# Performance work log

Hardware: AMD Instinct MI355X
Metric: run time of the kernel (lower is better)

The kernel has to match this reference:

```python
import jax, jax.numpy as jnp
import numpy as np

N_NODES = 100000
N_EDGES = 1600000
N_GRAPHS = 256
HIDDEN = 128
IN_FEAT = 5


def setup_inputs() -> dict:
    key = jax.random.key(0)
    ks = jax.random.split(key, 12)
    x = jax.random.normal(ks[0], (N_NODES, IN_FEAT), dtype=jnp.float32)
    edge_index = jax.random.randint(ks[1], (2, N_EDGES), 0, N_NODES, dtype=jnp.int64)
    batch = jnp.sort(jax.random.randint(ks[2], (N_NODES,), 0, N_GRAPHS, dtype=jnp.int64))
    s = 0.05
    W0 = jax.random.normal(ks[3], (IN_FEAT, HIDDEN), dtype=jnp.float32) * s
    b0 = jnp.zeros((HIDDEN,), dtype=jnp.float32)
    W1 = jax.random.normal(ks[4], (HIDDEN, HIDDEN), dtype=jnp.float32) * s
    b1 = jnp.zeros((HIDDEN,), dtype=jnp.float32)
    W2 = jax.random.normal(ks[5], (HIDDEN, HIDDEN), dtype=jnp.float32) * s
    b2 = jnp.zeros((HIDDEN,), dtype=jnp.float32)
    lin_w = jax.random.normal(ks[6], (HIDDEN, 1), dtype=jnp.float32) * s
    lin_b = jnp.zeros((1,), dtype=jnp.float32)
    return {"x": x, "edge_index": edge_index, "batch": batch,
            "W0": W0, "b0": b0, "W1": W1, "b1": b1, "W2": W2, "b2": b2,
            "lin_w": lin_w, "lin_b": lin_b}


def reference(x, edge_index, batch, W0, b0, W1, b1, W2, b2, lin_w, lin_b):
    n = x.shape[0]
    # PyG GCNConv: add self-loops, symmetric normalization D^-1/2 (A+I) D^-1/2
    loop = jnp.arange(n, dtype=edge_index.dtype)
    src = jnp.concatenate([edge_index[0], loop])  # [E+N]
    dst = jnp.concatenate([edge_index[1], loop])
    deg = jax.ops.segment_sum(jnp.ones_like(dst, dtype=x.dtype), dst, num_segments=n)
    dis = jnp.where(deg > 0, jax.lax.rsqrt(jnp.maximum(deg, 1.0)), 0.0)
    norm = (dis[src] * dis[dst])[:, None]  # [E+N, 1]

    def gcn_conv(h, W, b):
        h = h @ W                      # [N, H]
        msg = h[src] * norm            # gather + scale, [E+N, H]
        return jax.ops.segment_sum(msg, dst, num_segments=n) + b

    h = jax.nn.relu(gcn_conv(x, W0, b0))
    h = jax.nn.relu(gcn_conv(h, W1, b1))
    h = gcn_conv(h, W2, b2)

    # global_mean_pool over batch ids
    sums = jax.ops.segment_sum(h, batch, num_segments=N_GRAPHS)
    cnt = jax.ops.segment_sum(jnp.ones((n,), x.dtype), batch, num_segments=N_GRAPHS)
    g = sums / jnp.maximum(cnt, 1.0)[:, None]
    # dropout p=0.01 is identity in eval mode
    return jax.nn.sigmoid(g @ lin_w + lin_b)  # [N_GRAPHS, 1]
```

## Files before the change

### kernel.cpp

```cpp
#include <hip/hip_runtime.h>
#include <hip/hip_fp8.h>

#define GCN_N 100000
#define GCN_H 128
#define GCN_G 256
#define NPB_SHIFT 9
#define NPB 512
#define NBKT 196
#define CHUNK 2048
#define SRC_BITS 17
#define SRC_MASK ((1 << SRC_BITS) - 1)
#define T1_SCALE 256.0f
#define T1_INV_SCALE (1.0f / 256.0f)
#define EBUF_CAP 10240

static_assert(GCN_N < (1 << SRC_BITS), "src id must fit 17 bits");

using short8 = __attribute__((ext_vector_type(8))) short;
using f32x4  = __attribute__((ext_vector_type(4))) float;
using f32x2  = __attribute__((ext_vector_type(2))) float;

#if defined(__has_builtin)
#if __has_builtin(__builtin_amdgcn_cvt_pk_f32_fp8) && __has_builtin(__builtin_amdgcn_cvt_pk_fp8_f32)
#define HW_FP8 1
#endif
#endif


__device__ __forceinline__ unsigned short f2bf(float f) {
    unsigned u = __float_as_uint(f);
    unsigned r = u + 0x7FFFu + ((u >> 16) & 1u);
    return (unsigned short)(r >> 16);
}
__device__ __forceinline__ float bf2f(unsigned short h) {
    return __uint_as_float(((unsigned)h) << 16);
}

__device__ __forceinline__ void fp8x4_to_f32(unsigned v, float* f) {
#ifdef HW_FP8
    f32x2 lo = __builtin_amdgcn_cvt_pk_f32_fp8((int)v, false);
    f32x2 hi = __builtin_amdgcn_cvt_pk_f32_fp8((int)v, true);
    f[0] = lo[0]; f[1] = lo[1]; f[2] = hi[0]; f[3] = hi[1];
#else
    #pragma unroll
    for (int j = 0; j < 4; j++) {
        __hip_fp8_e4m3 h;
        h.__x = (unsigned char)((v >> (8 * j)) & 0xFF);
        f[j] = (float)h;
    }
#endif
}

__device__ __forceinline__ unsigned f32x4_to_fp8(float f0, float f1, float f2, float f3) {
#ifdef HW_FP8
    int r = __builtin_amdgcn_cvt_pk_fp8_f32(f0, f1, 0, false);
    r = __builtin_amdgcn_cvt_pk_fp8_f32(f2, f3, r, true);
    return (unsigned)r;
#else
    unsigned r = 0;
    float ff[4] = {f0, f1, f2, f3};
    #pragma unroll
    for (int j = 0; j < 4; j++) {
        __hip_fp8_e4m3 h(ff[j]);
        r |= ((unsigned)h.__x) << (8 * j);
    }
    return r;
#endif
}


__global__ __launch_bounds__(256) void hist_kernel(const int* __restrict__ dst,
                                                   int* __restrict__ hist, int E) {
    __shared__ int lh[NBKT];
    int tid = threadIdx.x;
    if (tid < NBKT) lh[tid] = 0;
    __syncthreads();
    int e0 = blockIdx.x * CHUNK;
    #pragma unroll
    for (int i = 0; i < CHUNK / 256; i++) {
        int e = e0 + tid + i * 256;
        if (e < E) atomicAdd(&lh[dst[e] >> NPB_SHIFT], 1);
    }
    __syncthreads();
    if (tid < NBKT) hist[(size_t)blockIdx.x * NBKT + tid] = lh[tid];
}

__global__ __launch_bounds__(64) void scan_cols_kernel(const int* __restrict__ hist,
                                                       int* __restrict__ offsT,
                                                       int* __restrict__ btot, int B) {
    int k = blockIdx.x;
    int lane = threadIdx.x;
    int running = 0;
    for (int b0 = 0; b0 < B; b0 += 64) {
        int b = b0 + lane;
        int v = (b < B) ? hist[(size_t)b * NBKT + k] : 0;
        int iv = v;
        #pragma unroll
        for (int d = 1; d < 64; d <<= 1) {
            int x = __shfl_up(iv, d, 64);
            if (lane >= d) iv += x;
        }
        if (b < B) offsT[(size_t)k * B + b] = running + iv - v;
        running += __shfl(iv, 63, 64);
    }
    if (lane == 0) btot[k] = running;
}

__global__ __launch_bounds__(256) void prep_kernel(const float* __restrict__ W1,
                                                   const float* __restrict__ W2,
                                                   const float* __restrict__ b2,
                                                   const float* __restrict__ lw,
                                                   const int* __restrict__ btot,
                                                   unsigned short* __restrict__ w1t,
                                                   float* __restrict__ w2l,
                                                   float* __restrict__ c2,
                                                   int* __restrict__ bbase,
                                                   int* __restrict__ rowptr, int n) {
    __shared__ float slw[128];
    int blk = blockIdx.x, tid = threadIdx.x;
    if (blk < 64) {
        int idx = blk * 256 + tid;
        int col = idx >> 7, k = idx & 127;
        w1t[idx] = f2bf(W1[k * 128 + col]);
    } else if (blk == 64) {
        if (tid < 128) slw[tid] = lw[tid];
        __syncthreads();
        if (tid < 128) {
            float s = 0.f;
            #pragma unroll 8
            for (int j = 0; j < 128; j++) s = fmaf(W2[tid * 128 + j], slw[j], s);
            w2l[tid] = s;
        } else if (tid == 128) {
            float s = 0.f;
            for (int j = 0; j < 128; j++) s = fmaf(b2[j], slw[j], s);
            c2[0] = s;
        }
    } else {
        if (tid == 0) {
            int run = 0;
            for (int i = 0; i < NBKT; i++) { bbase[i] = run; run += btot[i]; }
            bbase[NBKT] = run;
            rowptr[n] = run;
        }
    }
}

__global__ __launch_bounds__(256) void partition_kernel(const int* __restrict__ src,
                                                        const int* __restrict__ dst,
                                                        const int* __restrict__ bbase,
                                                        const int* __restrict__ offsT,
                                                        int* __restrict__ epack,
                                                        int E, int B) {
    __shared__ int cur[NBKT];
    int blk = blockIdx.x, tid = threadIdx.x;
    if (tid < NBKT) cur[tid] = bbase[tid] + offsT[(size_t)tid * B + blk];
    __syncthreads();
    int e0 = blk * CHUNK;
    #pragma unroll
    for (int i = 0; i < CHUNK / 256; i++) {
        int e = e0 + tid + i * 256;
        if (e < E) {
            int d = dst[e];
            int s = src[e];
            int pos = atomicAdd(&cur[d >> NPB_SHIFT], 1);
            epack[pos] = ((d & (NPB - 1)) << SRC_BITS) | s;
        }
    }
}

__global__ __launch_bounds__(512) void csr_build_kernel(const int* __restrict__ epack,
                                                        const int* __restrict__ bbase,
                                                        const float* __restrict__ x,
                                                        int* __restrict__ rowptr,
                                                        float* __restrict__ dis,
                                                        float* __restrict__ xsp,
                                                        int* __restrict__ csrc, int n) {
    __shared__ int ebuf[EBUF_CAP];
    __shared__ int lcount[NPB];
    __shared__ int lcur[NPB];
    __shared__ int wsums[8];
    int k = blockIdx.x, tid = threadIdx.x;
    int lane = tid & 63, wid = tid >> 6;
    int nodebase = k << NPB_SHIFT;
    int ebeg = bbase[k], eend = bbase[k + 1];
    bool fits = (eend - ebeg) <= EBUF_CAP;

    lcount[tid] = 0;
    __syncthreads();
    for (int e = ebeg + tid; e < eend; e += 512) {
        int p = epack[e];
        if (fits) ebuf[e - ebeg] = p;
        atomicAdd(&lcount[p >> SRC_BITS], 1);
    }
    __syncthreads();

    int v = lcount[tid];
    int iv = v;
    #pragma unroll
    for (int d = 1; d < 64; d <<= 1) {
        int x2 = __shfl_up(iv, d, 64);
        if (lane >= d) iv += x2;
    }
    if (lane == 63) wsums[wid] = iv;
    __syncthreads();
    if (tid == 0) {
        int r = 0;
        #pragma unroll
        for (int w = 0; w < 8; w++) { int t = wsums[w]; wsums[w] = r; r += t; }
    }
    __syncthreads();
    int ex = wsums[wid] + iv - v;
    lcur[tid] = ex;
    int node = nodebase + tid;
    if (node < n) {
        rowptr[node] = ebeg + ex;
        float dd = rsqrtf((float)(v + 1));
        dis[node] = dd;
        const float* xr = x + (size_t)node * 5;
        float4 a;
        a.x = xr[0] * dd; a.y = xr[1] * dd; a.z = xr[2] * dd; a.w = xr[3] * dd;
        float a4 = xr[4] * dd;
        ((float4*)(xsp + (size_t)node * 8))[0] = a;
        xsp[(size_t)node * 8 + 4] = a4;
        xsp[(size_t)node * 8 + 5] = 0.f;
        xsp[(size_t)node * 8 + 6] = 0.f;
        xsp[(size_t)node * 8 + 7] = 0.f;
    }
    __syncthreads();
    for (int e = ebeg + tid; e < eend; e += 512) {
        int p = fits ? ebuf[e - ebeg] : epack[e];
        int pos = atomicAdd(&lcur[p >> SRC_BITS], 1);
        csrc[ebeg + pos] = p & SRC_MASK;
    }
}


__global__ __launch_bounds__(256) void aggx_kernel(const float* __restrict__ xsp,
                                                   const float* __restrict__ dis,
                                                   const int* __restrict__ rowptr,
                                                   const int* __restrict__ csrc,
                                                   float* __restrict__ a0p, int n) {
    int i = blockIdx.x * 256 + threadIdx.x;
    if (i >= n) return;
    float4 acc = ((const float4*)(xsp + (size_t)i * 8))[0];
    float acc4 = xsp[(size_t)i * 8 + 4];
    int r0 = rowptr[i], r1 = rowptr[i + 1];
    int e = r0;
    for (; e + 7 < r1; e += 8) {
        int ss[8];
        #pragma unroll
        for (int u = 0; u < 8; u++) ss[u] = csrc[e + u];
        float4 v[8]; float a4[8];
        #pragma unroll
        for (int u = 0; u < 8; u++) {
            v[u] = ((const float4*)(xsp + (size_t)ss[u] * 8))[0];
            a4[u] = xsp[(size_t)ss[u] * 8 + 4];
        }
        #pragma unroll
        for (int u = 0; u < 8; u++) {
            acc.x += v[u].x; acc.y += v[u].y; acc.z += v[u].z; acc.w += v[u].w;
            acc4 += a4[u];
        }
    }
    for (; e < r1; e++) {
        int s = csrc[e];
        float4 v = ((const float4*)(xsp + (size_t)s * 8))[0];
        acc.x += v.x; acc.y += v.y; acc.z += v.z; acc.w += v.w;
        acc4 += xsp[(size_t)s * 8 + 4];
    }
    float di = dis[i];
    acc.x *= di; acc.y *= di; acc.z *= di; acc.w *= di; acc4 *= di;
    ((float4*)(a0p + (size_t)i * 8))[0] = acc;
    a0p[(size_t)i * 8 + 4] = acc4;
}


__global__ __launch_bounds__(256) void mmfused_kernel(const float* __restrict__ a0p,
                                                      const float* __restrict__ W0,
                                                      const float* __restrict__ b0,
                                                      const unsigned short* __restrict__ w1t,
                                                      const float* __restrict__ dis,
                                                      unsigned* __restrict__ t1f8, int n) {
    __shared__ __align__(16) unsigned short sA[128 * 128];
    __shared__ __align__(16) unsigned short sBT[128 * 128];
    __shared__ __align__(16) float4 sA0[256];
    __shared__ float sDis[128];
    char* sAb = (char*)sA;
    char* sBb = (char*)sBT;
    int tid = threadIdx.x;
    int rowBase = blockIdx.x * 128;

    {
        int rowL = tid >> 1, q = tid & 1;
        int gr = rowBase + rowL;
        float4 v = make_float4(0.f, 0.f, 0.f, 0.f);
        if (gr < n) v = ((const float4*)a0p)[(size_t)gr * 2 + q];
        sA0[tid] = v;
        if (tid < 128) {
            int g2 = rowBase + tid;
            sDis[tid] = (g2 < n) ? dis[g2] : 0.f;
        }
    }
    #pragma unroll
    for (int it = 0; it < 8; it++) {
        int idx = tid + it * 256;
        int col = idx >> 4, c = idx & 15;
        uint4 v = ((const uint4*)w1t)[idx];
        int byteoff = (col * 256 + c * 16) ^ ((col & 7) << 4);
        *(uint4*)(sBb + byteoff) = v;
    }
    __syncthreads();

    {
        int cq = tid & 31;
        int rg = tid >> 5;
        float4 w0q[5];
        #pragma unroll
        for (int j = 0; j < 5; j++) w0q[j] = *((const float4*)(W0 + j * 128 + cq * 4));
        float4 b0q = *((const float4*)(b0 + cq * 4));
        const float* sA0f = (const float*)sA0;
        #pragma unroll
        for (int ri = 0; ri < 16; ri++) {
            int row = rg + ri * 8;
            const float* ar = sA0f + row * 8;
            float4 h = b0q;
            #pragma unroll
            for (int j = 0; j < 5; j++) {
                float aj = ar[j];
                h.x = fmaf(aj, w0q[j].x, h.x);
                h.y = fmaf(aj, w0q[j].y, h.y);
                h.z = fmaf(aj, w0q[j].z, h.z);
                h.w = fmaf(aj, w0q[j].w, h.w);
            }
            h.x = fmaxf(h.x, 0.f); h.y = fmaxf(h.y, 0.f);
            h.z = fmaxf(h.z, 0.f); h.w = fmaxf(h.w, 0.f);
            uint2 p;
            p.x = (unsigned)f2bf(h.x) | ((unsigned)f2bf(h.y) << 16);
            p.y = (unsigned)f2bf(h.z) | ((unsigned)f2bf(h.w) << 16);
            int byteoff = (row * 256 + cq * 8) ^ ((row & 7) << 4);
            *(uint2*)(sAb + byteoff) = p;
        }
    }
    __syncthreads();

    int wave = tid >> 6, l = tid & 63;
    int lr = l & 15, lg = l >> 4;
    int rb = wave * 32;

    short8 afr[2][4];
    #pragma unroll
    for (int rt = 0; rt < 2; rt++) {
        int row = rb + rt * 16 + lr;
        #pragma unroll
        for (int ks = 0; ks < 4; ks++) {
            int byteoff = (row * 256 + ks * 64 + lg * 16) ^ ((row & 7) << 4);
            afr[rt][ks] = *(const short8*)(sAb + byteoff);
        }
    }
    f32x4 acc[2][8];
    #pragma unroll
    for (int rt = 0; rt < 2; rt++)
        #pragma unroll
        for (int ct = 0; ct < 8; ct++)
            acc[rt][ct] = (f32x4){0.f, 0.f, 0.f, 0.f};

    #pragma unroll
    for (int ct = 0; ct < 8; ct++) {
        int col = ct * 16 + lr;
        short8 bfr[4];
        #pragma unroll
        for (int ks = 0; ks < 4; ks++) {
            int byteoff = (col * 256 + ks * 64 + lg * 16) ^ ((col & 7) << 4);
            bfr[ks] = *(const short8*)(sBb + byteoff);
        }
        #pragma unroll
        for (int rt = 0; rt < 2; rt++) {
            #pragma unroll
            for (int ks = 0; ks < 4; ks++) {
                acc[rt][ct] = __builtin_amdgcn_mfma_f32_16x16x32_bf16(
                    afr[rt][ks], bfr[ks], acc[rt][ct], 0, 0, 0);
            }
        }
    }

    #pragma unroll
    for (int rt = 0; rt < 2; rt++) {
        #pragma unroll
        for (int i = 0; i < 4; i++) {
            int rowL = rb + rt * 16 + lg * 4 + i;
            float dsc = sDis[rowL] * T1_SCALE;
            #pragma unroll
            for (int ct = 0; ct < 8; ct++) {
                int col = ct * 16 + lr;
                int byteoff = (rowL * 256 + col * 2) ^ ((rowL & 7) << 4);
                *(unsigned short*)(sAb + byteoff) = f2bf(acc[rt][ct][i] * dsc);
            }
        }
    }
    __syncthreads();

    #pragma unroll
    for (int it = 0; it < 8; it++) {
        int flat = tid + it * 256;
        int rowL = flat >> 4, c16 = flat & 15;
        int gr = rowBase + rowL;
        if (gr < n) {
            int byteoff = (rowL * 256 + c16 * 16) ^ ((rowL & 7) << 4);
            uint4 v = *(const uint4*)(sAb + byteoff);
            float f0 = __uint_as_float(v.x << 16), f1 = __uint_as_float(v.x & 0xFFFF0000u);
            float f2 = __uint_as_float(v.y << 16), f3 = __uint_as_float(v.y & 0xFFFF0000u);
            float f4 = __uint_as_float(v.z << 16), f5 = __uint_as_float(v.z & 0xFFFF0000u);
            float f6 = __uint_as_float(v.w << 16), f7 = __uint_as_float(v.w & 0xFFFF0000u);
            uint2 p;
            p.x = f32x4_to_fp8(f0, f1, f2, f3);
            p.y = f32x4_to_fp8(f4, f5, f6, f7);
            ((uint2*)t1f8)[(size_t)gr * 16 + c16] = p;
        }
    }
}


__global__ __launch_bounds__(256) void agg1_kernel(const unsigned* __restrict__ t1f8,
                                                   const float* __restrict__ dis,
                                                   const int* __restrict__ rowptr,
                                                   const int* __restrict__ csrc,
                                                   const float* __restrict__ b1,
                                                   const float* __restrict__ w2l,
                                                   float* __restrict__ z, int n) {
    int group = threadIdx.x >> 4, lane = threadIdx.x & 15;
    int i = blockIdx.x * 16 + group;
    if (i >= n) return;
    const uint2* t2 = (const uint2*)t1f8;
    float f[8], acc[8];
    uint2 sv = t2[(size_t)i * 16 + lane];
    fp8x4_to_f32(sv.x, f);
    fp8x4_to_f32(sv.y, f + 4);
    #pragma unroll
    for (int j = 0; j < 8; j++) acc[j] = f[j];
    int r0 = rowptr[i], r1 = rowptr[i + 1];
    for (int e = r0; e < r1; e += 16) {
        int cnt = r1 - e; if (cnt > 16) cnt = 16;
        int idx = e + lane;
        int si = (idx < r1) ? csrc[idx] : 0;
        uint2 vv[16];
        #pragma unroll
        for (int u = 0; u < 16; u++) {
            if (u < cnt) {
                int s = __shfl(si, u, 16);
                vv[u] = t2[(size_t)s * 16 + lane];
            }
        }
        #pragma unroll
        for (int u = 0; u < 16; u++) {
            if (u < cnt) {
                fp8x4_to_f32(vv[u].x, f);
                fp8x4_to_f32(vv[u].y, f + 4);
                #pragma unroll
                for (int j = 0; j < 8; j++) acc[j] += f[j];
            }
        }
    }
    float di = dis[i];
    float dis_s = di * T1_INV_SCALE;
    float4 b4a = ((const float4*)b1)[lane * 2];
    float4 b4b = ((const float4*)b1)[lane * 2 + 1];
    float4 w4a = ((const float4*)w2l)[lane * 2];
    float4 w4b = ((const float4*)w2l)[lane * 2 + 1];
    float bb[8] = {b4a.x, b4a.y, b4a.z, b4a.w, b4b.x, b4b.y, b4b.z, b4b.w};
    float ww[8] = {w4a.x, w4a.y, w4a.z, w4a.w, w4b.x, w4b.y, w4b.z, w4b.w};
    float d = 0.f;
    #pragma unroll
    for (int j = 0; j < 8; j++) {
        float c = fmaxf(fmaf(dis_s, acc[j], bb[j]), 0.f);
        d = fmaf(c, ww[j], d);
    }
    #pragma unroll
    for (int o = 8; o > 0; o >>= 1) d += __shfl_down(d, o, 16);
    if (lane == 0) z[i] = di * d;
}


__global__ __launch_bounds__(256) void aggz_pool_kernel(const float* __restrict__ z,
                                                        const float* __restrict__ dis,
                                                        const int* __restrict__ rowptr,
                                                        const int* __restrict__ csrc,
                                                        const int* __restrict__ batch,
                                                        float* __restrict__ gsum,
                                                        int* __restrict__ gcnt, int n) {
    __shared__ float lg[GCN_G];
    __shared__ int lc[GCN_G];
    int tid = threadIdx.x;
    lg[tid] = 0.f;
    lc[tid] = 0;
    __syncthreads();
    int i = blockIdx.x * 256 + tid;
    bool valid = i < n;
    float ndv = 0.f;
    int g = 0;
    if (valid) {
        float acc = z[i];
        int r0 = rowptr[i], r1 = rowptr[i + 1];
        int e = r0;
        for (; e + 7 < r1; e += 8) {
            int ss[8];
            #pragma unroll
            for (int u = 0; u < 8; u++) ss[u] = csrc[e + u];
            float zv[8];
            #pragma unroll
            for (int u = 0; u < 8; u++) zv[u] = z[ss[u]];
            #pragma unroll
            for (int u = 0; u < 8; u++) acc += zv[u];
        }
        for (; e < r1; e++) acc += z[csrc[e]];
        ndv = dis[i] * acc;
        g = batch[i];
    }
    int lane = tid & 63;
    int g0 = __shfl(g, 0, 64);
    bool uni = __all(g == g0) && __all(valid);
    if (uni) {
        float s = ndv;
        #pragma unroll
        for (int o = 32; o > 0; o >>= 1) s += __shfl_down(s, o, 64);
        if (lane == 0) {
            atomicAdd(&lg[g0], s);
            atomicAdd(&lc[g0], 64);
        }
    } else if (valid) {
        atomicAdd(&lg[g], ndv);
        atomicAdd(&lc[g], 1);
    }
    __syncthreads();
    float v = lg[tid];
    int c = lc[tid];
    if (v != 0.f) atomicAdd(&gsum[tid], v);
    if (c != 0) atomicAdd(&gcnt[tid], c);
}


__global__ __launch_bounds__(256) void final_kernel(const float* __restrict__ gsum,
                                                    const int* __restrict__ gcnt,
                                                    const float* __restrict__ c2,
                                                    const float* __restrict__ lb,
                                                    float* __restrict__ out) {
    int g = threadIdx.x;
    float cnt = (float)max(gcnt[g], 1);
    float v = gsum[g] / cnt + c2[0] + lb[0];
    out[g] = 1.f / (1.f + expf(-v));
}


extern "C" void kernel_launch(void* const* d_in, const int* in_sizes, int n_in,
                              void* d_out, int out_size, void* d_ws, size_t ws_size,
                              hipStream_t stream) {
    const float* x   = (const float*)d_in[0];
    const int*   ei  = (const int*)d_in[1];
    const int*   bat = (const int*)d_in[2];
    const float* W0  = (const float*)d_in[3];
    const float* b0  = (const float*)d_in[4];
    const float* W1  = (const float*)d_in[5];
    const float* b1  = (const float*)d_in[6];
    const float* W2  = (const float*)d_in[7];
    const float* b2  = (const float*)d_in[8];
    const float* lw  = (const float*)d_in[9];
    const float* lb  = (const float*)d_in[10];
    float* out = (float*)d_out;

    const int N = GCN_N;
    const int E = in_sizes[1] / 2;
    const int B = (E + CHUNK - 1) / CHUNK;

    char* ws = (char*)d_ws;
    size_t off = 0;
    auto alloc = [&](size_t bytes) {
        size_t o = off;
        off += (bytes + 255) & ~(size_t)255;
        return o;
    };
    int*   hist    = (int*)(ws + alloc((size_t)B * NBKT * 4));
    int*   offsT   = (int*)(ws + alloc((size_t)NBKT * B * 4));
    int*   btot    = (int*)(ws + alloc((size_t)NBKT * 4));
    int*   bbase   = (int*)(ws + alloc((size_t)(NBKT + 1) * 4));
    int*   epack   = (int*)(ws + alloc((size_t)E * 4));
    int*   rowptr  = (int*)(ws + alloc((size_t)(N + 1) * 4));
    float* dis     = (float*)(ws + alloc((size_t)N * 4));
    int*   csrc    = (int*)(ws + alloc((size_t)E * 4));
    float* xsp     = (float*)(ws + alloc((size_t)N * 8 * 4));
    float* a0p     = (float*)(ws + alloc((size_t)N * 8 * 4));
    unsigned* t1f8 = (unsigned*)(ws + alloc((size_t)N * GCN_H));
    float* z       = (float*)(ws + alloc((size_t)N * 4));
    float* w2l     = (float*)(ws + alloc(128 * 4));
    float* c2      = (float*)(ws + alloc(4));
    unsigned short* w1t = (unsigned short*)(ws + alloc(128 * 128 * 2));
    float* gsum    = (float*)(ws + alloc(GCN_G * 4));
    int*   gcnt    = (int*)(ws + alloc(GCN_G * 4));

    const int* src = ei;
    const int* dst = ei + E;

    hipMemsetAsync(gsum, 0, GCN_G * 4 * 2, stream);

    hist_kernel<<<B, 256, 0, stream>>>(dst, hist, E);
    scan_cols_kernel<<<NBKT, 64, 0, stream>>>(hist, offsT, btot, B);
    prep_kernel<<<66, 256, 0, stream>>>(W1, W2, b2, lw, btot, w1t, w2l, c2, bbase, rowptr, N);
    partition_kernel<<<B, 256, 0, stream>>>(src, dst, bbase, offsT, epack, E, B);
    csr_build_kernel<<<NBKT, 512, 0, stream>>>(epack, bbase, x, rowptr, dis, xsp, csrc, N);

    aggx_kernel<<<(N + 255) / 256, 256, 0, stream>>>(xsp, dis, rowptr, csrc, a0p, N);
    mmfused_kernel<<<(N + 127) / 128, 256, 0, stream>>>(a0p, W0, b0, w1t, dis, t1f8, N);
    agg1_kernel<<<(N + 15) / 16, 256, 0, stream>>>(t1f8, dis, rowptr, csrc, b1, w2l, z, N);
    aggz_pool_kernel<<<(N + 255) / 256, 256, 0, stream>>>(z, dis, rowptr, csrc, bat, gsum, gcnt, N);

    final_kernel<<<1, 256, 0, stream>>>(gsum, gcnt, c2, lb, out);
}
```

Measured before the change: 149.6 us.

## Merge setup kernels and fold finalize via last-block tickets

The edge histogram and the weight prep now run in one kernel. The bucket-base scan moves into scan_cols through a last-block ticket counter, and the final sigmoid moves into the pool kernel the same way, so two kernel launches disappear. agg1 also prefetches the next batch of CSR source indices while the current gathers are in flight. The ticket counters need zeroing each call, which the enlarged memset does, and the last-block pattern depends on threadfence ordering being correct.

Result: slower. 175.6 us (+17.4%).

```diff
diff --git a/kernel.cpp b/kernel.cpp
--- a/kernel.cpp
+++ b/kernel.cpp
@@ -69,60 +69,34 @@
 }
 
 
-__global__ __launch_bounds__(256) void hist_kernel(const int* __restrict__ dst,
-                                                   int* __restrict__ hist, int E) {
+__global__ __launch_bounds__(256) void hist_prep_kernel(const int* __restrict__ dst,
+                                                        int* __restrict__ hist, int E, int B,
+                                                        const float* __restrict__ W1,
+                                                        const float* __restrict__ W2,
+                                                        const float* __restrict__ b2,
+                                                        const float* __restrict__ lw,
+                                                        unsigned short* __restrict__ w1t,
+                                                        float* __restrict__ w2l,
+                                                        float* __restrict__ c2) {
     __shared__ int lh[NBKT];
-    int tid = threadIdx.x;
-    if (tid < NBKT) lh[tid] = 0;
-    __syncthreads();
-    int e0 = blockIdx.x * CHUNK;
-    #pragma unroll
-    for (int i = 0; i < CHUNK / 256; i++) {
-        int e = e0 + tid + i * 256;
-        if (e < E) atomicAdd(&lh[dst[e] >> NPB_SHIFT], 1);
-    }
-    __syncthreads();
-    if (tid < NBKT) hist[(size_t)blockIdx.x * NBKT + tid] = lh[tid];
-}
-
-__global__ __launch_bounds__(64) void scan_cols_kernel(const int* __restrict__ hist,
-                                                       int* __restrict__ offsT,
-                                                       int* __restrict__ btot, int B) {
-    int k = blockIdx.x;
-    int lane = threadIdx.x;
-    int running = 0;
-    for (int b0 = 0; b0 < B; b0 += 64) {
-        int b = b0 + lane;
-        int v = (b < B) ? hist[(size_t)b * NBKT + k] : 0;
-        int iv = v;
-        #pragma unroll
-        for (int d = 1; d < 64; d <<= 1) {
-            int x = __shfl_up(iv, d, 64);
-            if (lane >= d) iv += x;
-        }
-        if (b < B) offsT[(size_t)k * B + b] = running + iv - v;
-        running += __shfl(iv, 63, 64);
-    }
-    if (lane == 0) btot[k] = running;
-}
-
-__global__ __launch_bounds__(256) void prep_kernel(const float* __restrict__ W1,
-                                                   const float* __restrict__ W2,
-                                                   const float* __restrict__ b2,
-                                                   const float* __restrict__ lw,
-                                                   const int* __restrict__ btot,
-                                                   unsigned short* __restrict__ w1t,
-                                                   float* __restrict__ w2l,
-                                                   float* __restrict__ c2,
-                                                   int* __restrict__ bbase,
-                                                   int* __restrict__ rowptr, int n) {
     __shared__ float slw[128];
     int blk = blockIdx.x, tid = threadIdx.x;
-    if (blk < 64) {
-        int idx = blk * 256 + tid;
+    if (blk < B) {
+        if (tid < NBKT) lh[tid] = 0;
+        __syncthreads();
+        int e0 = blk * CHUNK;
+        #pragma unroll
+        for (int i = 0; i < CHUNK / 256; i++) {
+            int e = e0 + tid + i * 256;
+            if (e < E) atomicAdd(&lh[dst[e] >> NPB_SHIFT], 1);
+        }
+        __syncthreads();
+        if (tid < NBKT) hist[(size_t)blk * NBKT + tid] = lh[tid];
+    } else if (blk < B + 64) {
+        int idx = (blk - B) * 256 + tid;
         int col = idx >> 7, k = idx & 127;
         w1t[idx] = f2bf(W1[k * 128 + col]);
-    } else if (blk == 64) {
+    } else {
         if (tid < 128) slw[tid] = lw[tid];
         __syncthreads();
         if (tid < 128) {
@@ -135,13 +109,52 @@
             for (int j = 0; j < 128; j++) s = fmaf(b2[j], slw[j], s);
             c2[0] = s;
         }
-    } else {
-        if (tid == 0) {
-            int run = 0;
-            for (int i = 0; i < NBKT; i++) { bbase[i] = run; run += btot[i]; }
-            bbase[NBKT] = run;
-            rowptr[n] = run;
-        }
+    }
+}
+
+__global__ __launch_bounds__(64) void scan_cols_kernel(const int* __restrict__ hist,
+                                                       int* __restrict__ offsT,
+                                                       int* __restrict__ btot,
+                                                       int* __restrict__ bbase,
+                                                       int* __restrict__ rowptr,
+                                                       int* __restrict__ done2,
+                                                       int B, int n) {
+    __shared__ int stick;
+    int k = blockIdx.x;
+    int lane = threadIdx.x;
+    int running = 0;
+    for (int b0 = 0; b0 < B; b0 += 64) {
+        int b = b0 + lane;
+        int v = (b < B) ? hist[(size_t)b * NBKT + k] : 0;
+        int iv = v;
+        #pragma unroll
+        for (int d = 1; d < 64; d <<= 1) {
+            int x = __shfl_up(iv, d, 64);
+            if (lane >= d) iv += x;
+        }
+        if (b < B) offsT[(size_t)k * B + b] = running + iv - v;
+        running += __shfl(iv, 63, 64);
+    }
+    if (lane == 0) btot[k] = running;
+    __threadfence();
+    if (lane == 0) stick = atomicAdd(done2, 1);
+    __syncthreads();
+    if (stick == NBKT - 1) {
+        __threadfence();
+        int run = 0;
+        for (int b0 = 0; b0 < NBKT; b0 += 64) {
+            int kk = b0 + lane;
+            int v = (kk < NBKT) ? atomicAdd(&btot[kk], 0) : 0;
+            int iv = v;
+            #pragma unroll
+            for (int d = 1; d < 64; d <<= 1) {
+                int x = __shfl_up(iv, d, 64);
+                if (lane >= d) iv += x;
+            }
+            if (kk < NBKT) bbase[kk] = run + iv - v;
+            run += __shfl(iv, 63, 64);
+        }
+        if (lane == 0) { bbase[NBKT] = run; rowptr[n] = run; }
     }
 }
 
@@ -438,10 +451,10 @@
     #pragma unroll
     for (int j = 0; j < 8; j++) acc[j] = f[j];
     int r0 = rowptr[i], r1 = rowptr[i + 1];
-    for (int e = r0; e < r1; e += 16) {
+    int e = r0;
+    int si = (e + lane < r1) ? csrc[e + lane] : 0;
+    while (e < r1) {
         int cnt = r1 - e; if (cnt > 16) cnt = 16;
-        int idx = e + lane;
-        int si = (idx < r1) ? csrc[idx] : 0;
         uint2 vv[16];
         #pragma unroll
         for (int u = 0; u < 16; u++) {
@@ -450,6 +463,8 @@
                 vv[u] = t2[(size_t)s * 16 + lane];
             }
         }
+        int e2 = e + 16;
+        int si2 = (e2 + lane < r1) ? csrc[e2 + lane] : 0;
         #pragma unroll
         for (int u = 0; u < 16; u++) {
             if (u < cnt) {
@@ -459,6 +474,7 @@
                 for (int j = 0; j < 8; j++) acc[j] += f[j];
             }
         }
+        si = si2; e = e2;
     }
     float di = dis[i];
     float dis_s = di * T1_INV_SCALE;
@@ -485,10 +501,15 @@
                                                         const int* __restrict__ rowptr,
                                                         const int* __restrict__ csrc,
                                                         const int* __restrict__ batch,
+                                                        const float* __restrict__ c2,
+                                                        const float* __restrict__ lb,
                                                         float* __restrict__ gsum,
-                                                        int* __restrict__ gcnt, int n) {
+                                                        int* __restrict__ gcnt,
+                                                        int* __restrict__ done,
+                                                        float* __restrict__ out, int n) {
     __shared__ float lg[GCN_G];
     __shared__ int lc[GCN_G];
+    __shared__ int sticket;
     int tid = threadIdx.x;
     lg[tid] = 0.f;
     lc[tid] = 0;
@@ -535,18 +556,16 @@
     int c = lc[tid];
     if (v != 0.f) atomicAdd(&gsum[tid], v);
     if (c != 0) atomicAdd(&gcnt[tid], c);
-}
-
-
-__global__ __launch_bounds__(256) void final_kernel(const float* __restrict__ gsum,
-                                                    const int* __restrict__ gcnt,
-                                                    const float* __restrict__ c2,
-                                                    const float* __restrict__ lb,
-                                                    float* __restrict__ out) {
-    int g = threadIdx.x;
-    float cnt = (float)max(gcnt[g], 1);
-    float v = gsum[g] / cnt + c2[0] + lb[0];
-    out[g] = 1.f / (1.f + expf(-v));
+
+    __threadfence();
+    if (tid == 0) sticket = atomicAdd(done, 1);
+    __syncthreads();
+    if (sticket == (int)gridDim.x - 1) {
+        float sv = atomicAdd(&gsum[tid], 0.f);
+        int cv = atomicAdd(&gcnt[tid], 0);
+        float vv = sv / (float)max(cv, 1) + c2[0] + lb[0];
+        out[tid] = 1.f / (1.f + expf(-vv));
+    }
 }
 
 
@@ -594,22 +613,22 @@
     unsigned short* w1t = (unsigned short*)(ws + alloc(128 * 128 * 2));
     float* gsum    = (float*)(ws + alloc(GCN_G * 4));
     int*   gcnt    = (int*)(ws + alloc(GCN_G * 4));
+    int*   done    = (int*)(ws + alloc(4));
+    int*   done2   = (int*)(ws + alloc(4));
 
     const int* src = ei;
     const int* dst = ei + E;
 
-    hipMemsetAsync(gsum, 0, GCN_G * 4 * 2, stream);
-
-    hist_kernel<<<B, 256, 0, stream>>>(dst, hist, E);
-    scan_cols_kernel<<<NBKT, 64, 0, stream>>>(hist, offsT, btot, B);
-    prep_kernel<<<66, 256, 0, stream>>>(W1, W2, b2, lw, btot, w1t, w2l, c2, bbase, rowptr, N);
+    hipMemsetAsync(gsum, 0, GCN_G * 4 * 2 + 512, stream);
+
+    hist_prep_kernel<<<B + 65, 256, 0, stream>>>(dst, hist, E, B, W1, W2, b2, lw, w1t, w2l, c2);
+    scan_cols_kernel<<<NBKT, 64, 0, stream>>>(hist, offsT, btot, bbase, rowptr, done2, B, N);
     partition_kernel<<<B, 256, 0, stream>>>(src, dst, bbase, offsT, epack, E, B);
     csr_build_kernel<<<NBKT, 512, 0, stream>>>(epack, bbase, x, rowptr, dis, xsp, csrc, N);
 
     aggx_kernel<<<(N + 255) / 256, 256, 0, stream>>>(xsp, dis, rowptr, csrc, a0p, N);
     mmfused_kernel<<<(N + 127) / 128, 256, 0, stream>>>(a0p, W0, b0, w1t, dis, t1f8, N);
     agg1_kernel<<<(N + 15) / 16, 256, 0, stream>>>(t1f8, dis, rowptr, csrc, b1, w2l, z, N);
-    aggz_pool_kernel<<<(N + 255) / 256, 256, 0, stream>>>(z, dis, rowptr, csrc, bat, gsum, gcnt, N);
-
-    final_kernel<<<1, 256, 0, stream>>>(gsum, gcnt, c2, lb, out);
-}
+    aggz_pool_kernel<<<(N + 255) / 256, 256, 0, stream>>>(z, dis, rowptr, csrc, bat, c2, lb,
+                                                          gsum, gcnt, done, out, N);
+}
```
